# Kernel tuning notes

Measured on AMD Instinct MI355X. Metric: run time of the kernel, lower is better.

Reference implementation:

```python
import jax, jax.numpy as jnp
import numpy as np

QB = 127.0  # 2**(8-1) - 1
LN_EPS = 1e-5


def _bitlinear(x, W):
    # LayerNorm (no affine)
    mu = jnp.mean(x, axis=-1, keepdims=True)
    var = jnp.mean((x - mu) ** 2, axis=-1, keepdims=True)
    xn = (x - mu) * jax.lax.rsqrt(var + LN_EPS)
    # per-tensor absmax activation fake-quant with STE
    eps = jnp.finfo(x.dtype).eps
    gamma = jnp.maximum(jnp.max(jnp.abs(xn)), 1e-8)
    xs = xn * (QB / gamma)
    xq_hard = jnp.round(jnp.clip(xs, -QB + eps, QB - eps))
    xq = xn + jax.lax.stop_gradient(xq_hard - xn)
    # binary weight quant: sign(W - mean(W)) with STE, scale beta = mean(|W|)
    alpha = jnp.mean(W)
    beta = jnp.maximum(jnp.mean(jnp.abs(W)), 1e-8)
    ws = W - alpha
    wb = ws + jax.lax.stop_gradient(jnp.where(ws > 0, 1.0, -1.0).astype(W.dtype) - ws)
    out = xq @ wb.T  # [B, out_features]
    return out * (beta * gamma / QB)


def setup_inputs() -> dict:
    key = jax.random.key(0)
    k0, k1, k2, k3 = jax.random.split(key, 4)
    B, D_IN, D_H, D_OUT = 131072, 256, 256, 256
    x = jax.random.normal(k0, (B, D_IN), dtype=jnp.float32)
    W1 = jax.random.normal(k1, (D_H, D_IN), dtype=jnp.float32) * 0.02
    W2 = jax.random.normal(k2, (D_H, D_H), dtype=jnp.float32) * 0.02
    W3 = jax.random.normal(k3, (D_OUT, D_H), dtype=jnp.float32) * 0.02
    return {"x": x, "W1": W1, "W2": W2, "W3": W3}


def reference(x, W1, W2, W3):
    h = jax.nn.relu(_bitlinear(x, W1))
    h = jax.nn.relu(_bitlinear(h, W2))
    return _bitlinear(h, W3)
```

## Files before the change

kernel.cpp:

```cpp
#include <hip/hip_runtime.h>
#include <stdint.h>

#define NROWS 131072
#define DIM 256

typedef __attribute__((ext_vector_type(4))) float f32x4;
typedef __attribute__((ext_vector_type(8))) __bf16 bf16x8;
typedef __attribute__((ext_vector_type(4))) short s16x4;
typedef __attribute__((ext_vector_type(8))) short s16x8;

__device__ __forceinline__ short bftrunc(float f) {
  return (short)(__float_as_uint(f) >> 16);
}

__device__ __forceinline__ void gload_lds16(const unsigned short* g, unsigned short* lds) {
  __builtin_amdgcn_global_load_lds((const __attribute__((address_space(1))) void*)g,
                                   (__attribute__((address_space(3))) void*)lds, 16, 0, 0);
}

__global__ __launch_bounds__(256) void k_stats(const float* __restrict__ x,
                                               float* __restrict__ mu_o, float* __restrict__ rs_o,
                                               unsigned* __restrict__ gslot) {
  const int l = threadIdx.x & 63;
  const int gw = blockIdx.x * 4 + (threadIdx.x >> 6);
  float gmax = 0.f;
  for (int i = 0; i < 16; ++i) {
    const int row = gw * 16 + i;
    f32x4 v = *(const f32x4*)(x + (size_t)row * DIM + l * 4);
    float s = v.x + v.y + v.z + v.w;
    #pragma unroll
    for (int m = 1; m < 64; m <<= 1) s += __shfl_xor(s, m);
    const float mu = s * (1.f / 256.f);
    float d0 = v.x - mu, d1 = v.y - mu, d2 = v.z - mu, d3 = v.w - mu;
    float sq = d0 * d0 + d1 * d1 + d2 * d2 + d3 * d3;
    float am = fmaxf(fmaxf(fabsf(d0), fabsf(d1)), fmaxf(fabsf(d2), fabsf(d3)));
    #pragma unroll
    for (int m = 1; m < 64; m <<= 1) {
      sq += __shfl_xor(sq, m);
      am = fmaxf(am, __shfl_xor(am, m));
    }
    const float rstd = rsqrtf(sq * (1.f / 256.f) + 1e-5f);
    if (l == 0) { mu_o[row] = mu; rs_o[row] = rstd; }
    gmax = fmaxf(gmax, am * rstd);
  }
  if (l == 0) atomicMax(gslot + (gw & 63), __float_as_uint(gmax));
}

__global__ __launch_bounds__(256) void k_wstats1(const float* __restrict__ W0,
                                                 const float* __restrict__ W1,
                                                 const float* __restrict__ W2,
                                                 float2* __restrict__ part) {
  const int layer = blockIdx.y;
  const float* W = layer == 0 ? W0 : (layer == 1 ? W1 : W2);
  const int idx = (blockIdx.x * 256 + threadIdx.x) * 4;
  f32x4 v = *(const f32x4*)(W + idx);
  float s = v.x + v.y + v.z + v.w;
  float sa = fabsf(v.x) + fabsf(v.y) + fabsf(v.z) + fabsf(v.w);
  #pragma unroll
  for (int m = 1; m < 64; m <<= 1) { s += __shfl_xor(s, m); sa += __shfl_xor(sa, m); }
  __shared__ float bs[4], ba[4];
  const int w = threadIdx.x >> 6, l = threadIdx.x & 63;
  if (l == 0) { bs[w] = s; ba[w] = sa; }
  __syncthreads();
  if (threadIdx.x == 0) {
    float2 p;
    p.x = bs[0] + bs[1] + bs[2] + bs[3];
    p.y = ba[0] + ba[1] + ba[2] + ba[3];
    part[layer * 64 + blockIdx.x] = p;
  }
}

__global__ __launch_bounds__(64) void k_wstats2(const float2* __restrict__ part,
                                                float* __restrict__ ab) {
  const int layer = blockIdx.x;
  float2 p = part[layer * 64 + threadIdx.x];
  float s = p.x, sa = p.y;
  #pragma unroll
  for (int m = 1; m < 64; m <<= 1) { s += __shfl_xor(s, m); sa += __shfl_xor(sa, m); }
  if (threadIdx.x == 0) {
    ab[layer] = s * (1.f / 65536.f);
    ab[3 + layer] = fmaxf(sa * (1.f / 65536.f), 1e-8f);
  }
}

__global__ __launch_bounds__(256) void k_pack(const float* __restrict__ W0,
                                              const float* __restrict__ W1,
                                              const float* __restrict__ W2,
                                              const float* __restrict__ ab,
                                              unsigned short* __restrict__ bp) {
  const int layer = blockIdx.y;
  const float* W = layer == 0 ? W0 : (layer == 1 ? W1 : W2);
  const float alpha = ab[layer];
  const int p = blockIdx.x * 256 + threadIdx.x;
  const int r = p & 7, l = (p >> 3) & 63, nt = (p >> 9) & 15, kt = p >> 13;
  const int k = kt * 32 + ((l >> 4) << 3) + r;
  const int j = nt * 16 + (l & 15);
  bp[layer * 65536 + p] = (W[j * 256 + k] > alpha) ? 0x3F80u : 0xBF80u;
}

template <int FINAL>
__global__ __launch_bounds__(256, 2) void k_gemm(
    const float* src, const float* __restrict__ mu, const float* __restrict__ rs,
    const unsigned* __restrict__ gslot, const unsigned short* __restrict__ bp,
    const float* __restrict__ beta_p,
    float* __restrict__ hout, float* bout,
    float* __restrict__ mu_n, float* __restrict__ rs_n, unsigned* __restrict__ gslot_n) {
  __shared__ unsigned short Ab[128][72];
  __shared__ unsigned short Bb[16384];
  __shared__ float smu[128], srs[128], sg[1];

  const int t = threadIdx.x, l = t & 63, w = t >> 6;
  const int row0 = blockIdx.x * 128;

  if (t < 128) {
    smu[t] = mu[row0 + t];
    srs[t] = rs[row0 + t];
  } else if (t >= 192) {
    float g = __uint_as_float(gslot[t - 192]);
    #pragma unroll
    for (int m = 1; m < 64; m <<= 1) g = fmaxf(g, __shfl_xor(g, m));
    if (t == 192) sg[0] = fmaxf(g, 1e-8f);
  }
  __syncthreads();
  const float gamma = sg[0];
  const float qs = 127.f / gamma;
  const float beta = *beta_p;
  const float oscale = beta * gamma * (1.f / 127.f);

  f32x4 acc[2][16];
  #pragma unroll
  for (int mt = 0; mt < 2; ++mt)
    #pragma unroll
    for (int i = 0; i < 16; ++i) acc[mt][i] = (f32x4){0.f, 0.f, 0.f, 0.f};

  const int ar = t >> 1, ah = t & 1;
  const float c1 = srs[ar] * qs;
  const float c0 = -smu[ar] * c1;

  for (int s = 0; s < 4; ++s) {
    {
      const unsigned short* bps = bp + s * 16384 + l * 8;
      #pragma unroll
      for (int it = 0; it < 8; ++it) {
        const int c = (w * 8 + it) * 512;
        gload_lds16(bps + c, &Bb[c]);
      }
    }
    {
      const float* px = src + (size_t)(row0 + ar) * DIM + s * 64 + ah * 32;
      #pragma unroll
      for (int jj = 0; jj < 8; ++jj) {
        f32x4 v = *(const f32x4*)(px + jj * 4);
        s16x4 q;
        #pragma unroll
        for (int e = 0; e < 4; ++e) {
          float xs = __builtin_fmaf(v[e], c1, c0);
          xs = fminf(fmaxf(xs, -127.f), 127.f);
          q[e] = bftrunc(rintf(xs));
        }
        *(s16x4*)&Ab[ar][ah * 32 + jj * 4] = q;
      }
    }
    __syncthreads();
    #pragma unroll
    for (int kt2 = 0; kt2 < 2; ++kt2) {
      bf16x8 aF[2];
      #pragma unroll
      for (int mt = 0; mt < 2; ++mt)
        aF[mt] = *(const bf16x8*)&Ab[(w << 5) + (mt << 4) + (l & 15)][kt2 * 32 + ((l >> 4) << 3)];
      #pragma unroll
      for (int nt = 0; nt < 16; ++nt) {
        bf16x8 b = *(const bf16x8*)&Bb[((kt2 * 16 + nt) * 64 + l) * 8];
        acc[0][nt] = __builtin_amdgcn_mfma_f32_16x16x32_bf16(aF[0], b, acc[0][nt], 0, 0, 0);
        acc[1][nt] = __builtin_amdgcn_mfma_f32_16x16x32_bf16(aF[1], b, acc[1][nt], 0, 0, 0);
      }
    }
    __syncthreads();
  }

  const int colb = l & 15;
  const int g = l >> 4;

  if constexpr (FINAL == 1) {
    #pragma unroll
    for (int mt = 0; mt < 2; ++mt)
      #pragma unroll
      for (int nt = 0; nt < 16; ++nt)
        #pragma unroll
        for (int rr = 0; rr < 4; ++rr) {
          const int grow = row0 + (w << 5) + (mt << 4) + (g << 2) + rr;
          bout[(size_t)grow * DIM + nt * 16 + colb] = acc[mt][nt][rr] * oscale;
        }
  } else {
    float gmax = 0.f;
    #pragma unroll
    for (int mt = 0; mt < 2; ++mt) {
      float sum[4] = {0.f, 0.f, 0.f, 0.f};
      #pragma unroll
      for (int nt = 0; nt < 16; ++nt)
        #pragma unroll
        for (int rr = 0; rr < 4; ++rr) {
          float h = fmaxf(acc[mt][nt][rr] * oscale, 0.f);
          acc[mt][nt][rr] = h;
          sum[rr] += h;
          hout[(size_t)(row0 + (w << 5) + (mt << 4) + (g << 2) + rr) * DIM + nt * 16 + colb] = h;
        }
      #pragma unroll
      for (int rr = 0; rr < 4; ++rr) {
        float s_ = sum[rr];
        s_ += __shfl_xor(s_, 1); s_ += __shfl_xor(s_, 2);
        s_ += __shfl_xor(s_, 4); s_ += __shfl_xor(s_, 8);
        const float m_ = s_ * (1.f / 256.f);
        float sq = 0.f, am = 0.f;
        #pragma unroll
        for (int nt = 0; nt < 16; ++nt) {
          float d = acc[mt][nt][rr] - m_;
          sq += d * d;
          am = fmaxf(am, fabsf(d));
        }
        sq += __shfl_xor(sq, 1); sq += __shfl_xor(sq, 2);
        sq += __shfl_xor(sq, 4); sq += __shfl_xor(sq, 8);
        am = fmaxf(am, __shfl_xor(am, 1)); am = fmaxf(am, __shfl_xor(am, 2));
        am = fmaxf(am, __shfl_xor(am, 4)); am = fmaxf(am, __shfl_xor(am, 8));
        const float rstd = rsqrtf(sq * (1.f / 256.f) + 1e-5f);
        const int grow = row0 + (w << 5) + (mt << 4) + (g << 2) + rr;
        if (colb == 0) { mu_n[grow] = m_; rs_n[grow] = rstd; }
        gmax = fmaxf(gmax, am * rstd);
      }
    }
    gmax = fmaxf(gmax, __shfl_xor(gmax, 16));
    gmax = fmaxf(gmax, __shfl_xor(gmax, 32));
    if (l == 0) atomicMax(gslot_n + (blockIdx.x & 63), __float_as_uint(gmax));
  }
}

extern "C" void kernel_launch(void* const* d_in, const int* in_sizes, int n_in,
                              void* d_out, int out_size, void* d_ws, size_t ws_size,
                              hipStream_t stream) {
  const float* x  = (const float*)d_in[0];
  const float* W1 = (const float*)d_in[1];
  const float* W2 = (const float*)d_in[2];
  const float* W3 = (const float*)d_in[3];

  char* ws = (char*)d_ws;
  unsigned* gslot = (unsigned*)ws;
  float* ab = (float*)(ws + 1024);
  float2* part = (float2*)(ws + 2048);
  float* muv = (float*)(ws + 4096);
  float* rsv = (float*)(ws + 4096 + 3 * 524288);
  unsigned short* bp = (unsigned short*)(ws + 3149824);
  float* h1 = (float*)(ws + 4194304);
  float* h2 = (float*)d_out;

  hipMemsetAsync(gslot, 0, 768, stream);
  dim3 wg(64, 3);
  k_wstats1<<<wg, 256, 0, stream>>>(W1, W2, W3, part);
  k_wstats2<<<3, 64, 0, stream>>>(part, ab);
  dim3 pg(256, 3);
  k_pack<<<pg, 256, 0, stream>>>(W1, W2, W3, ab, bp);
  k_stats<<<2048, 256, 0, stream>>>(x, muv, rsv, gslot);

  k_gemm<0><<<1024, 256, 0, stream>>>(x, muv, rsv, gslot, bp, ab + 3,
                                      h1, nullptr,
                                      muv + 131072, rsv + 131072, gslot + 64);
  k_gemm<0><<<1024, 256, 0, stream>>>(h1, muv + 131072, rsv + 131072, gslot + 64,
                                      bp + 65536, ab + 4,
                                      h2, nullptr,
                                      muv + 262144, rsv + 262144, gslot + 128);
  k_gemm<1><<<1024, 256, 0, stream>>>(h2, muv + 262144, rsv + 262144, gslot + 128,
                                      bp + 131072, ab + 5,
                                      nullptr, (float*)d_out,
                                      nullptr, nullptr, nullptr);
}
```

Before: 442.7 us.

## Drop LDS staging in GEMM; load A fragments and packed B directly from global

Removes the shared-memory tiles for A and B and the block-wide barriers. Each wave now loads its own fp32 activation rows straight into MFMA fragment registers, quantizes them in-register, and reads pre-packed binary weights directly from global memory (L2/L1 cached). It also computes quantization as (x-mu)*rs*qs instead of one fma, and the weight pack subtracts alpha before comparing. This cuts LDS traffic and synchronization, but the B matrix is re-read per wave from cache and the strided activation loads may coalesce less well.

```diff
diff --git a/kernel.cpp b/kernel.cpp
--- a/kernel.cpp
+++ b/kernel.cpp
@@ -5,17 +5,12 @@
 #define DIM 256
 
 typedef __attribute__((ext_vector_type(4))) float f32x4;
+typedef __attribute__((ext_vector_type(8))) float f32x8;
 typedef __attribute__((ext_vector_type(8))) __bf16 bf16x8;
-typedef __attribute__((ext_vector_type(4))) short s16x4;
 typedef __attribute__((ext_vector_type(8))) short s16x8;
 
 __device__ __forceinline__ short bftrunc(float f) {
   return (short)(__float_as_uint(f) >> 16);
-}
-
-__device__ __forceinline__ void gload_lds16(const unsigned short* g, unsigned short* lds) {
-  __builtin_amdgcn_global_load_lds((const __attribute__((address_space(1))) void*)g,
-                                   (__attribute__((address_space(3))) void*)lds, 16, 0, 0);
 }
 
 __global__ __launch_bounds__(256) void k_stats(const float* __restrict__ x,
@@ -95,7 +90,8 @@
   const int r = p & 7, l = (p >> 3) & 63, nt = (p >> 9) & 15, kt = p >> 13;
   const int k = kt * 32 + ((l >> 4) << 3) + r;
   const int j = nt * 16 + (l & 15);
-  bp[layer * 65536 + p] = (W[j * 256 + k] > alpha) ? 0x3F80u : 0xBF80u;
+  const float wv = W[j * 256 + k] - alpha;
+  bp[layer * 65536 + p] = (wv > 0.f) ? 0x3F80u : 0xBF80u;
 }
 
 template <int FINAL>
@@ -105,81 +101,54 @@
     const float* __restrict__ beta_p,
     float* __restrict__ hout, float* bout,
     float* __restrict__ mu_n, float* __restrict__ rs_n, unsigned* __restrict__ gslot_n) {
-  __shared__ unsigned short Ab[128][72];
-  __shared__ unsigned short Bb[16384];
-  __shared__ float smu[128], srs[128], sg[1];
-
   const int t = threadIdx.x, l = t & 63, w = t >> 6;
-  const int row0 = blockIdx.x * 128;
-
-  if (t < 128) {
-    smu[t] = mu[row0 + t];
-    srs[t] = rs[row0 + t];
-  } else if (t >= 192) {
-    float g = __uint_as_float(gslot[t - 192]);
-    #pragma unroll
-    for (int m = 1; m < 64; m <<= 1) g = fmaxf(g, __shfl_xor(g, m));
-    if (t == 192) sg[0] = fmaxf(g, 1e-8f);
-  }
-  __syncthreads();
-  const float gamma = sg[0];
+  const int row0 = blockIdx.x * 128 + w * 32;
+  const int lr = l & 15, g2 = l >> 4;
+
+  float gm = __uint_as_float(gslot[l]);
+  #pragma unroll
+  for (int m = 1; m < 64; m <<= 1) gm = fmaxf(gm, __shfl_xor(gm, m));
+  const float gamma = fmaxf(gm, 1e-8f);
   const float qs = 127.f / gamma;
   const float beta = *beta_p;
   const float oscale = beta * gamma * (1.f / 127.f);
 
+  const float mu0 = mu[row0 + lr],      rs0 = rs[row0 + lr];
+  const float mu1 = mu[row0 + 16 + lr], rs1 = rs[row0 + 16 + lr];
+
   f32x4 acc[2][16];
   #pragma unroll
   for (int mt = 0; mt < 2; ++mt)
     #pragma unroll
     for (int i = 0; i < 16; ++i) acc[mt][i] = (f32x4){0.f, 0.f, 0.f, 0.f};
 
-  const int ar = t >> 1, ah = t & 1;
-  const float c1 = srs[ar] * qs;
-  const float c0 = -smu[ar] * c1;
-
-  for (int s = 0; s < 4; ++s) {
-    {
-      const unsigned short* bps = bp + s * 16384 + l * 8;
-      #pragma unroll
-      for (int it = 0; it < 8; ++it) {
-        const int c = (w * 8 + it) * 512;
-        gload_lds16(bps + c, &Bb[c]);
-      }
-    }
-    {
-      const float* px = src + (size_t)(row0 + ar) * DIM + s * 64 + ah * 32;
-      #pragma unroll
-      for (int jj = 0; jj < 8; ++jj) {
-        f32x4 v = *(const f32x4*)(px + jj * 4);
-        s16x4 q;
-        #pragma unroll
-        for (int e = 0; e < 4; ++e) {
-          float xs = __builtin_fmaf(v[e], c1, c0);
-          xs = fminf(fmaxf(xs, -127.f), 127.f);
-          q[e] = bftrunc(rintf(xs));
-        }
-        *(s16x4*)&Ab[ar][ah * 32 + jj * 4] = q;
-      }
-    }
-    __syncthreads();
-    #pragma unroll
-    for (int kt2 = 0; kt2 < 2; ++kt2) {
-      bf16x8 aF[2];
-      #pragma unroll
-      for (int mt = 0; mt < 2; ++mt)
-        aF[mt] = *(const bf16x8*)&Ab[(w << 5) + (mt << 4) + (l & 15)][kt2 * 32 + ((l >> 4) << 3)];
-      #pragma unroll
-      for (int nt = 0; nt < 16; ++nt) {
-        bf16x8 b = *(const bf16x8*)&Bb[((kt2 * 16 + nt) * 64 + l) * 8];
-        acc[0][nt] = __builtin_amdgcn_mfma_f32_16x16x32_bf16(aF[0], b, acc[0][nt], 0, 0, 0);
-        acc[1][nt] = __builtin_amdgcn_mfma_f32_16x16x32_bf16(aF[1], b, acc[1][nt], 0, 0, 0);
-      }
-    }
-    __syncthreads();
-  }
-
-  const int colb = l & 15;
-  const int g = l >> 4;
+  const float* a0p = src + (size_t)(row0 + lr) * DIM + g2 * 8;
+  const float* a1p = a0p + 16 * DIM;
+  const unsigned short* bpl = bp + l * 8;
+
+  #pragma unroll
+  for (int c = 0; c < 8; ++c) {
+    f32x8 v0 = *(const f32x8*)(a0p + c * 32);
+    f32x8 v1 = *(const f32x8*)(a1p + c * 32);
+    union { s16x8 s; bf16x8 b; } a0u, a1u;
+    #pragma unroll
+    for (int e = 0; e < 8; ++e) {
+      float xn = (v0[e] - mu0) * rs0;
+      float xs = xn * qs;
+      xs = fminf(fmaxf(xs, -127.f), 127.f);
+      a0u.s[e] = bftrunc(rintf(xs));
+      float yn = (v1[e] - mu1) * rs1;
+      float ys = yn * qs;
+      ys = fminf(fmaxf(ys, -127.f), 127.f);
+      a1u.s[e] = bftrunc(rintf(ys));
+    }
+    #pragma unroll
+    for (int nt = 0; nt < 16; ++nt) {
+      bf16x8 b = *(const bf16x8*)(bpl + (c * 16 + nt) * 512);
+      acc[0][nt] = __builtin_amdgcn_mfma_f32_16x16x32_bf16(a0u.b, b, acc[0][nt], 0, 0, 0);
+      acc[1][nt] = __builtin_amdgcn_mfma_f32_16x16x32_bf16(a1u.b, b, acc[1][nt], 0, 0, 0);
+    }
+  }
 
   if constexpr (FINAL == 1) {
     #pragma unroll
@@ -188,8 +157,8 @@
       for (int nt = 0; nt < 16; ++nt)
         #pragma unroll
         for (int rr = 0; rr < 4; ++rr) {
-          const int grow = row0 + (w << 5) + (mt << 4) + (g << 2) + rr;
-          bout[(size_t)grow * DIM + nt * 16 + colb] = acc[mt][nt][rr] * oscale;
+          const int grow = row0 + mt * 16 + g2 * 4 + rr;
+          bout[(size_t)grow * DIM + nt * 16 + lr] = acc[mt][nt][rr] * oscale;
         }
   } else {
     float gmax = 0.f;
@@ -203,7 +172,7 @@
           float h = fmaxf(acc[mt][nt][rr] * oscale, 0.f);
           acc[mt][nt][rr] = h;
           sum[rr] += h;
-          hout[(size_t)(row0 + (w << 5) + (mt << 4) + (g << 2) + rr) * DIM + nt * 16 + colb] = h;
+          hout[(size_t)(row0 + mt * 16 + g2 * 4 + rr) * DIM + nt * 16 + lr] = h;
         }
       #pragma unroll
       for (int rr = 0; rr < 4; ++rr) {
@@ -223,8 +192,8 @@
         am = fmaxf(am, __shfl_xor(am, 1)); am = fmaxf(am, __shfl_xor(am, 2));
         am = fmaxf(am, __shfl_xor(am, 4)); am = fmaxf(am, __shfl_xor(am, 8));
         const float rstd = rsqrtf(sq * (1.f / 256.f) + 1e-5f);
-        const int grow = row0 + (w << 5) + (mt << 4) + (g << 2) + rr;
-        if (colb == 0) { mu_n[grow] = m_; rs_n[grow] = rstd; }
+        const int grow = row0 + mt * 16 + g2 * 4 + rr;
+        if (lr == 0) { mu_n[grow] = m_; rs_n[grow] = rstd; }
         gmax = fmaxf(gmax, am * rstd);
       }
     }
```

New measurement: 538.7 us. 21.7% more time.
